# Performance work log

Hardware: AMD Instinct MI355X
Metric: run time of the kernel (lower is better)

Reference implementation:

```python
import jax, jax.numpy as jnp
import numpy as np

B = 131072  # batch size; feature dims 256->64->16->4 are hardcoded in the module


def setup_inputs() -> dict:
    key = jax.random.key(0)
    ks = jax.random.split(key, 7)
    return {
        "x": jax.random.normal(ks[0], (B, 256), dtype=jnp.float32),
        "w1": jax.random.normal(ks[1], (256, 64), dtype=jnp.float32),
        "b1": jax.random.normal(ks[2], (1, 64), dtype=jnp.float32),
        "w2": jax.random.normal(ks[3], (64, 16), dtype=jnp.float32),
        "b2": jax.random.normal(ks[4], (1, 16), dtype=jnp.float32),
        "w3": jax.random.normal(ks[5], (16, 4), dtype=jnp.float32),
        "b3": jax.random.normal(ks[6], (1, 4), dtype=jnp.float32),
    }


def reference(x, w1, b1, w2, b2, w3, b3):
    h = jax.nn.relu(x @ w1 + b1)          # [B, 64]
    h = jnp.tanh(h @ w2 + b2)             # [B, 16]
    logits = h @ w3 + b3                  # [B, 4]
    # Faithful to original soft(): softmax over the ENTIRE flattened tensor
    # (normalizes across batch AND class dims), then reshape back.
    y = jax.nn.softmax(logits.reshape(-1)).reshape(logits.shape)
    return y
```

## Files before the change

kernel.cpp:

```cpp
#include <hip/hip_runtime.h>
#include <hip/hip_bf16.h>
#include <math.h>


typedef __attribute__((ext_vector_type(8))) short bf16x8;
typedef __attribute__((ext_vector_type(4))) float f32x4;

#define WK 520
#define HS 68
#define NBLOCKS 512

__device__ __forceinline__ short f2bf(float v) {
    unsigned u = __float_as_uint(v);
    unsigned r = (u + 0x7FFFu + ((u >> 16) & 1u)) >> 16;
    return (short)r;
}
__device__ __forceinline__ float bf2f(short s) {
    return __uint_as_float(((unsigned)(unsigned short)s) << 16);
}

__device__ __forceinline__ void cvt8(const float4 v0, const float4 v1,
                                     bf16x8& ah, bf16x8& al)
{
    const float f[8] = {v0.x, v0.y, v0.z, v0.w, v1.x, v1.y, v1.z, v1.w};
    unsigned* ahp = (unsigned*)&ah;
    unsigned* alp = (unsigned*)&al;
#pragma unroll
    for (int p = 0; p < 4; ++p) {
        float2 fp = make_float2(f[2 * p], f[2 * p + 1]);
        __hip_bfloat162 h2 = __float22bfloat162_rn(fp);
        float2 hf = __bfloat1622float2(h2);
        __hip_bfloat162 l2 =
            __float22bfloat162_rn(make_float2(fp.x - hf.x, fp.y - hf.y));
        union { __hip_bfloat162 b; unsigned u; } ch, cl;
        ch.b = h2; cl.b = l2;
        ahp[p] = ch.u;
        alp[p] = cl.u;
    }
}

__global__ __launch_bounds__(512, 4)
void mlp_kernel(const float* __restrict__ x, const float* __restrict__ w1,
                const float* __restrict__ b1, const float* __restrict__ w2,
                const float* __restrict__ b2, const float* __restrict__ w3,
                const float* __restrict__ b3, float* __restrict__ out,
                float* __restrict__ wsum)
{
    __shared__ __align__(16) char smem[256 * HS * 4];
    __shared__ float ws2[64 * 16];
    __shared__ float ws3[64];
    __shared__ float bs1[64];
    __shared__ float bsum[8];
    short* wlds = (short*)smem;
    float* hs   = (float*)smem;

    const int tid  = threadIdx.x;
    const int lane = tid & 63;
    const int wid  = tid >> 6;
    const int quad = lane >> 4;
    const int m16  = lane & 15;

    for (int i = tid; i < 1024; i += 512) ws2[i] = w2[i];
    if (tid < 64) ws3[tid] = w3[tid];
    if (tid >= 64 && tid < 128) bs1[tid - 64] = b1[tid - 64];
    {
        const int n  = tid & 63;
        const int kb = (tid >> 6) * 4;
        for (int kk = kb; kk < 256; kk += 32) {
            const float v0 = w1[(size_t)(kk + 0) * 64 + n];
            const float v1 = w1[(size_t)(kk + 1) * 64 + n];
            const float v2 = w1[(size_t)(kk + 2) * 64 + n];
            const float v3 = w1[(size_t)(kk + 3) * 64 + n];
            short4 hi, lo;
            hi.x = f2bf(v0); lo.x = f2bf(v0 - bf2f(hi.x));
            hi.y = f2bf(v1); lo.y = f2bf(v1 - bf2f(hi.y));
            hi.z = f2bf(v2); lo.z = f2bf(v2 - bf2f(hi.z));
            hi.w = f2bf(v3); lo.w = f2bf(v3 - bf2f(hi.w));
            *(short4*)&wlds[n * WK + kk]       = hi;
            *(short4*)&wlds[n * WK + 256 + kk] = lo;
        }
    }
    __syncthreads();

    const int row0 = blockIdx.x * 256 + wid * 32;
    const float* xb0 = x + (size_t)(row0 + m16) * 256 + quad * 8;
    const float* xb1 = xb0 + 16 * 256;

    f32x4 acc[2][4];
#pragma unroll
    for (int mt = 0; mt < 2; ++mt)
#pragma unroll
        for (int t = 0; t < 4; ++t) acc[mt][t] = (f32x4)0.0f;

    float4 cur[4];
    cur[0] = *(const float4*)(xb0);
    cur[1] = *(const float4*)(xb0 + 4);
    cur[2] = *(const float4*)(xb1);
    cur[3] = *(const float4*)(xb1 + 4);

#pragma unroll
    for (int s = 0; s < 8; ++s) {
        float4 nxt[4];
        if (s < 7) {
            const int off = (s + 1) * 32;
            nxt[0] = *(const float4*)(xb0 + off);
            nxt[1] = *(const float4*)(xb0 + off + 4);
            nxt[2] = *(const float4*)(xb1 + off);
            nxt[3] = *(const float4*)(xb1 + off + 4);
        }
        bf16x8 bh[4], bl[4];
#pragma unroll
        for (int t = 0; t < 4; ++t) {
            const short* bp = &wlds[(t * 16 + m16) * WK + s * 32 + quad * 8];
            bh[t] = *(const bf16x8*)bp;
            bl[t] = *(const bf16x8*)(bp + 256);
        }
#pragma unroll
        for (int mt = 0; mt < 2; ++mt) {
            bf16x8 ah, al;
            cvt8(cur[mt * 2 + 0], cur[mt * 2 + 1], ah, al);
#pragma unroll
            for (int t = 0; t < 4; ++t)
                acc[mt][t] = __builtin_amdgcn_mfma_f32_16x16x32_bf16(
                    ah, bh[t], acc[mt][t], 0, 0, 0);
#pragma unroll
            for (int t = 0; t < 4; ++t)
                acc[mt][t] = __builtin_amdgcn_mfma_f32_16x16x32_bf16(
                    al, bh[t], acc[mt][t], 0, 0, 0);
#pragma unroll
            for (int t = 0; t < 4; ++t)
                acc[mt][t] = __builtin_amdgcn_mfma_f32_16x16x32_bf16(
                    ah, bl[t], acc[mt][t], 0, 0, 0);
        }
#pragma unroll
        for (int i = 0; i < 4; ++i) cur[i] = nxt[i];
    }
    __syncthreads();

#pragma unroll
    for (int mt = 0; mt < 2; ++mt)
#pragma unroll
        for (int t = 0; t < 4; ++t) {
            const float bc = bs1[t * 16 + m16];
#pragma unroll
            for (int r = 0; r < 4; ++r) {
                const int rr = wid * 32 + mt * 16 + quad * 4 + r;
                hs[rr * HS + t * 16 + m16] = fmaxf(acc[mt][t][r] + bc, 0.0f);
            }
        }
    __syncthreads();

    const int r2 = tid >> 1;
    const int jq = (tid & 1) * 8;
    float z2[8];
#pragma unroll
    for (int jj = 0; jj < 8; ++jj) z2[jj] = b2[jq + jj];
#pragma unroll 4
    for (int c = 0; c < 64; c += 4) {
        const float4 h4 = *(const float4*)&hs[r2 * HS + c];
        const float hv[4] = {h4.x, h4.y, h4.z, h4.w};
#pragma unroll
        for (int i = 0; i < 4; ++i)
#pragma unroll
            for (int jj = 0; jj < 8; ++jj)
                z2[jj] = fmaf(hv[i], ws2[(c + i) * 16 + jq + jj], z2[jj]);
    }
    float l0 = 0.f, l1 = 0.f, l2 = 0.f, l3 = 0.f;
#pragma unroll
    for (int jj = 0; jj < 8; ++jj) {
        const float th = tanhf(z2[jj]);
        const int j = jq + jj;
        l0 = fmaf(th, ws3[j * 4 + 0], l0);
        l1 = fmaf(th, ws3[j * 4 + 1], l1);
        l2 = fmaf(th, ws3[j * 4 + 2], l2);
        l3 = fmaf(th, ws3[j * 4 + 3], l3);
    }
    l0 += __shfl_xor(l0, 1); l1 += __shfl_xor(l1, 1);
    l2 += __shfl_xor(l2, 1); l3 += __shfl_xor(l3, 1);

    float s = 0.0f;
    if ((tid & 1) == 0) {
        const float e0 = expf(l0 + b3[0]);
        const float e1 = expf(l1 + b3[1]);
        const float e2 = expf(l2 + b3[2]);
        const float e3 = expf(l3 + b3[3]);
        *(float4*)&out[(size_t)(blockIdx.x * 256 + r2) * 4] =
            make_float4(e0, e1, e2, e3);
        s = e0 + e1 + e2 + e3;
    }
#pragma unroll
    for (int off = 1; off < 64; off <<= 1) s += __shfl_xor(s, off);
    if (lane == 0) bsum[wid] = s;
    __syncthreads();
    if (tid == 0) {
        float tot = 0.0f;
#pragma unroll
        for (int i = 0; i < 8; ++i) tot += bsum[i];
        atomicAdd(wsum, tot);
    }
}

__global__ __launch_bounds__(256)
void norm_kernel(float4* __restrict__ out, const float* __restrict__ wsum, int n4)
{
    const int i = blockIdx.x * 256 + threadIdx.x;
    if (i < n4) {
        const float inv = 1.0f / *wsum;
        float4 v = out[i];
        v.x *= inv; v.y *= inv; v.z *= inv; v.w *= inv;
        out[i] = v;
    }
}

extern "C" void kernel_launch(void* const* d_in, const int* in_sizes, int n_in,
                              void* d_out, int out_size, void* d_ws, size_t ws_size,
                              hipStream_t stream) {
    (void)in_sizes; (void)n_in; (void)ws_size;
    const float* x  = (const float*)d_in[0];
    const float* w1 = (const float*)d_in[1];
    const float* b1 = (const float*)d_in[2];
    const float* w2 = (const float*)d_in[3];
    const float* b2 = (const float*)d_in[4];
    const float* w3 = (const float*)d_in[5];
    const float* b3 = (const float*)d_in[6];
    float* out  = (float*)d_out;
    float* wsum = (float*)d_ws;

    hipMemsetAsync(wsum, 0, sizeof(float), stream);
    mlp_kernel<<<NBLOCKS, 512, 0, stream>>>(x, w1, b1, w2, b2, w3, b3, out, wsum);
    const int n4 = out_size >> 2;
    norm_kernel<<<(n4 + 255) / 256, 256, 0, stream>>>((float4*)out, wsum, n4);
}
```

Baseline: 216.7 us.

## Stage x tiles through double-buffered LDS with coalesced row loads

Input rows are now loaded with a coalesced pattern (8 lanes per 128-byte row segment) into a double-buffered shared-memory tile, instead of each lane reading scattered 32-byte pieces directly in MFMA fragment layout. Fragments are then read from LDS, with a barrier per k-step to swap buffers. The goal is better global-memory coalescing. In exchange it uses much more LDS (occupancy hint lowered from 4 to 2 blocks) and adds seven block-wide syncs per block.

New measurement: 225.0 us. 1.04x slower.

```diff
diff --git a/kernel.cpp b/kernel.cpp
--- a/kernel.cpp
+++ b/kernel.cpp
@@ -6,8 +6,9 @@
 typedef __attribute__((ext_vector_type(8))) short bf16x8;
 typedef __attribute__((ext_vector_type(4))) float f32x4;
 
-#define WK 520
-#define HS 68
+#define WKD 260
+#define XS  36
+#define HSS 68
 #define NBLOCKS 512
 
 __device__ __forceinline__ short f2bf(float v) {
@@ -39,26 +40,42 @@
     }
 }
 
-__global__ __launch_bounds__(512, 4)
+__global__ __launch_bounds__(512, 2)
 void mlp_kernel(const float* __restrict__ x, const float* __restrict__ w1,
                 const float* __restrict__ b1, const float* __restrict__ w2,
                 const float* __restrict__ b2, const float* __restrict__ w3,
                 const float* __restrict__ b3, float* __restrict__ out,
                 float* __restrict__ wsum)
 {
-    __shared__ __align__(16) char smem[256 * HS * 4];
+    __shared__ __align__(16) short wlds[64 * 2 * WKD];
+    __shared__ __align__(16) float xbuf[2][256 * XS];
     __shared__ float ws2[64 * 16];
     __shared__ float ws3[64];
     __shared__ float bs1[64];
     __shared__ float bsum[8];
-    short* wlds = (short*)smem;
-    float* hs   = (float*)smem;
+    float* hs = xbuf[0];
 
     const int tid  = threadIdx.x;
     const int lane = tid & 63;
     const int wid  = tid >> 6;
     const int quad = lane >> 4;
     const int m16  = lane & 15;
+    const int row0 = blockIdx.x * 256;
+
+    const int srow = lane >> 3;
+    const int scol = (lane & 7) * 4;
+    const float* gx[4];
+    int lx[4];
+#pragma unroll
+    for (int q = 0; q < 4; ++q) {
+        const int rl = wid * 32 + q * 8 + srow;
+        gx[q] = x + (size_t)(row0 + rl) * 256 + scol;
+        lx[q] = rl * XS + scol;
+    }
+
+    float4 pre[4];
+#pragma unroll
+    for (int q = 0; q < 4; ++q) pre[q] = *(const float4*)(gx[q]);
 
     for (int i = tid; i < 1024; i += 512) ws2[i] = w2[i];
     if (tid < 64) ws3[tid] = w3[tid];
@@ -76,15 +93,14 @@
             hi.y = f2bf(v1); lo.y = f2bf(v1 - bf2f(hi.y));
             hi.z = f2bf(v2); lo.z = f2bf(v2 - bf2f(hi.z));
             hi.w = f2bf(v3); lo.w = f2bf(v3 - bf2f(hi.w));
-            *(short4*)&wlds[n * WK + kk]       = hi;
-            *(short4*)&wlds[n * WK + 256 + kk] = lo;
-        }
-    }
-    __syncthreads();
-
-    const int row0 = blockIdx.x * 256 + wid * 32;
-    const float* xb0 = x + (size_t)(row0 + m16) * 256 + quad * 8;
-    const float* xb1 = xb0 + 16 * 256;
+            short* wrow = wlds + n * 2 * WKD;
+            *(short4*)&wrow[kk]       = hi;
+            *(short4*)&wrow[256 + kk] = lo;
+        }
+    }
+#pragma unroll
+    for (int q = 0; q < 4; ++q) *(float4*)&xbuf[0][lx[q]] = pre[q];
+    __syncthreads();
 
     f32x4 acc[2][4];
 #pragma unroll
@@ -92,33 +108,31 @@
 #pragma unroll
         for (int t = 0; t < 4; ++t) acc[mt][t] = (f32x4)0.0f;
 
-    float4 cur[4];
-    cur[0] = *(const float4*)(xb0);
-    cur[1] = *(const float4*)(xb0 + 4);
-    cur[2] = *(const float4*)(xb1);
-    cur[3] = *(const float4*)(xb1 + 4);
-
 #pragma unroll
     for (int s = 0; s < 8; ++s) {
-        float4 nxt[4];
+        const int b = s & 1;
+        float4 nx[4];
         if (s < 7) {
-            const int off = (s + 1) * 32;
-            nxt[0] = *(const float4*)(xb0 + off);
-            nxt[1] = *(const float4*)(xb0 + off + 4);
-            nxt[2] = *(const float4*)(xb1 + off);
-            nxt[3] = *(const float4*)(xb1 + off + 4);
-        }
+#pragma unroll
+            for (int q = 0; q < 4; ++q)
+                nx[q] = *(const float4*)(gx[q] + (s + 1) * 32);
+        }
+
         bf16x8 bh[4], bl[4];
 #pragma unroll
         for (int t = 0; t < 4; ++t) {
-            const short* bp = &wlds[(t * 16 + m16) * WK + s * 32 + quad * 8];
+            const short* bp = wlds + (t * 16 + m16) * 2 * WKD
+                                   + s * 32 + quad * 8;
             bh[t] = *(const bf16x8*)bp;
             bl[t] = *(const bf16x8*)(bp + 256);
         }
 #pragma unroll
         for (int mt = 0; mt < 2; ++mt) {
+            const float* xp = &xbuf[b][(wid * 32 + mt * 16 + m16) * XS + quad * 8];
+            const float4 v0 = *(const float4*)xp;
+            const float4 v1 = *(const float4*)(xp + 4);
             bf16x8 ah, al;
-            cvt8(cur[mt * 2 + 0], cur[mt * 2 + 1], ah, al);
+            cvt8(v0, v1, ah, al);
 #pragma unroll
             for (int t = 0; t < 4; ++t)
                 acc[mt][t] = __builtin_amdgcn_mfma_f32_16x16x32_bf16(
@@ -132,8 +146,13 @@
                 acc[mt][t] = __builtin_amdgcn_mfma_f32_16x16x32_bf16(
                     ah, bl[t], acc[mt][t], 0, 0, 0);
         }
-#pragma unroll
-        for (int i = 0; i < 4; ++i) cur[i] = nxt[i];
+
+        if (s < 7) {
+#pragma unroll
+            for (int q = 0; q < 4; ++q)
+                *(float4*)&xbuf[1 - b][lx[q]] = nx[q];
+            __syncthreads();
+        }
     }
     __syncthreads();
 
@@ -145,7 +164,7 @@
 #pragma unroll
             for (int r = 0; r < 4; ++r) {
                 const int rr = wid * 32 + mt * 16 + quad * 4 + r;
-                hs[rr * HS + t * 16 + m16] = fmaxf(acc[mt][t][r] + bc, 0.0f);
+                hs[rr * HSS + t * 16 + m16] = fmaxf(acc[mt][t][r] + bc, 0.0f);
             }
         }
     __syncthreads();
@@ -157,7 +176,7 @@
     for (int jj = 0; jj < 8; ++jj) z2[jj] = b2[jq + jj];
 #pragma unroll 4
     for (int c = 0; c < 64; c += 4) {
-        const float4 h4 = *(const float4*)&hs[r2 * HS + c];
+        const float4 h4 = *(const float4*)&hs[r2 * HSS + c];
         const float hv[4] = {h4.x, h4.y, h4.z, h4.w};
 #pragma unroll
         for (int i = 0; i < 4; ++i)
@@ -184,7 +203,7 @@
         const float e1 = expf(l1 + b3[1]);
         const float e2 = expf(l2 + b3[2]);
         const float e3 = expf(l3 + b3[3]);
-        *(float4*)&out[(size_t)(blockIdx.x * 256 + r2) * 4] =
+        *(float4*)&out[(size_t)(row0 + r2) * 4] =
             make_float4(e0, e1, e2, e3);
         s = e0 + e1 + e2 + e3;
     }
```
